# Performance work log

Hardware: AMD Instinct MI355X
Metric: run time of the kernel (lower is better)

Reference implementation:

```python
import jax, jax.numpy as jnp
import numpy as np

B, H, S, D = 2, 16, 2048, 64
DILATION_RATE = 2

def dilated_global_mask(seq_len: int, dilation_rate: int) -> jnp.ndarray:
    # mask[i, j] = 1 if |i - j| % dilation_rate == 0 else 0  -> [S, S] float32
    i = jnp.arange(seq_len)[:, None]
    j = jnp.arange(seq_len)[None, :]
    return ((jnp.abs(i - j) % dilation_rate) == 0).astype(jnp.float32)

def setup_inputs() -> dict:
    key = jax.random.key(0)
    kq, kk, kv = jax.random.split(key, 3)
    queries = jax.random.normal(kq, (B, H, S, D), dtype=jnp.float32)
    keys = jax.random.normal(kk, (B, H, S, D), dtype=jnp.float32)
    values = jax.random.normal(kv, (B, H, S, D), dtype=jnp.float32)
    return {"queries": queries, "keys": keys, "values": values}

def reference(queries, keys, values):
    depth = queries.shape[-1]
    # scores: [B, H, S, S]
    scores = jnp.einsum("bhqd,bhkd->bhqk", queries, keys)
    scores = scores / jnp.sqrt(jnp.asarray(depth, dtype=jnp.float32))
    gmask = dilated_global_mask(keys.shape[-2], DILATION_RATE)  # [S, S]
    # NOTE: multiplicative masking (masked scores become 0, not -inf), as in source
    masked_scores = scores * gmask
    attention_probs = jax.nn.softmax(masked_scores, axis=-1)
    # dropout is identity at inference (training=None)
    out = jnp.einsum("bhqk,bhkd->bhqd", attention_probs, values)
    return out
```

## Files before the change

kernel.cpp:

```cpp
#include <hip/hip_runtime.h>
#include <hip/hip_bf16.h>


#define B_   2
#define H_   16
#define S_   2048
#define D_   64
#define SP_  1024
#define BQ   128
#define BK   64
#define NKT  (SP_ / BK)

#define QSCALE 0.180336884f

typedef __bf16 bf16x8 __attribute__((ext_vector_type(8)));
typedef float  f32x4  __attribute__((ext_vector_type(4)));

#define KSW(r, c8) ((((c8) ^ ((r) & 7)) << 3))

__global__ __launch_bounds__(256, 2) void attn_kernel(const float* __restrict__ Q,
                                                      const float* __restrict__ K,
                                                      const float* __restrict__ V,
                                                      float* __restrict__ out) {
    const int bh  = blockIdx.x;
    const int par = blockIdx.y;
    const int qt  = blockIdx.z;
    const int tid  = threadIdx.x;
    const int lane = tid & 63;
    const int wave = tid >> 6;
    const int l15  = lane & 15;
    const int quad = lane >> 4;

    __shared__ __align__(16) __bf16 kbuf[2][BK][64];
    __shared__ __align__(16) __bf16 vbuf[2][D_][64];
    __shared__ __align__(16) __bf16 p_s[4][16][64];

    const size_t base = (size_t)bh * S_ * D_;
    const float* Qb = Q + base;
    const float* Kb = K + base;
    const float* Vb = V + base;
    const int vofs = (par == 0) ? D_ : -D_;

    bf16x8 qf[2][2];
    #pragma unroll
    for (int mt = 0; mt < 2; ++mt) {
        const int qrow = qt * BQ + wave * 32 + mt * 16 + l15;
        const float* qsrc = Qb + (size_t)(par + 2 * qrow) * D_ + quad * 8;
        #pragma unroll
        for (int ks = 0; ks < 2; ++ks) {
            const float4 a = *(const float4*)(qsrc + ks * 32);
            const float4 b = *(const float4*)(qsrc + ks * 32 + 4);
            bf16x8 w;
            w[0] = (__bf16)(a.x * QSCALE); w[1] = (__bf16)(a.y * QSCALE);
            w[2] = (__bf16)(a.z * QSCALE); w[3] = (__bf16)(a.w * QSCALE);
            w[4] = (__bf16)(b.x * QSCALE); w[5] = (__bf16)(b.y * QSCALE);
            w[6] = (__bf16)(b.z * QSCALE); w[7] = (__bf16)(b.w * QSCALE);
            qf[mt][ks] = w;
        }
    }

    const int kr0 = tid >> 3;
    const int kc8 = tid & 7;

    float4 pka[2], pkb[2];
    float  pv[16], pvo[16];

    #pragma unroll
    for (int i = 0; i < 2; ++i) {
        const int r = i * 32 + kr0;
        const float* ksrc = Kb + (size_t)(par + 2 * r) * D_ + kc8 * 8;
        pka[i] = *(const float4*)ksrc;
        pkb[i] = *(const float4*)(ksrc + 4);
    }
    #pragma unroll
    for (int i = 0; i < 2; ++i) {
        const int c = wave + 4 * i;
        const float* vsrc = Vb + (size_t)(par + 2 * (c * 8)) * D_ + lane;
        #pragma unroll
        for (int j = 0; j < 8; ++j) {
            pv [i * 8 + j] = vsrc[(size_t)(2 * j) * D_];
            pvo[i * 8 + j] = vsrc[(size_t)(2 * j) * D_ + vofs];
        }
    }

    float vo = 0.f;
    #pragma unroll
    for (int i = 0; i < 2; ++i) {
        const int r = i * 32 + kr0;
        bf16x8 w;
        w[0] = (__bf16)pka[i].x; w[1] = (__bf16)pka[i].y;
        w[2] = (__bf16)pka[i].z; w[3] = (__bf16)pka[i].w;
        w[4] = (__bf16)pkb[i].x; w[5] = (__bf16)pkb[i].y;
        w[6] = (__bf16)pkb[i].z; w[7] = (__bf16)pkb[i].w;
        *(bf16x8*)&kbuf[0][r][KSW(r, kc8)] = w;
    }
    #pragma unroll
    for (int i = 0; i < 2; ++i) {
        const int c = wave + 4 * i;
        bf16x8 w;
        #pragma unroll
        for (int j = 0; j < 8; ++j) w[j] = (__bf16)pv[i * 8 + j];
        *(bf16x8*)&vbuf[0][lane][KSW(lane, c)] = w;
        vo += ((pvo[i*8+0] + pvo[i*8+1]) + (pvo[i*8+2] + pvo[i*8+3]))
            + ((pvo[i*8+4] + pvo[i*8+5]) + (pvo[i*8+6] + pvo[i*8+7]));
    }
    __syncthreads();

    f32x4 acc[2][4];
    #pragma unroll
    for (int mt = 0; mt < 2; ++mt)
        #pragma unroll
        for (int nt = 0; nt < 4; ++nt) acc[mt][nt] = (f32x4){0.f, 0.f, 0.f, 0.f};
    float l_acc[2][4] = {{0.f,0.f,0.f,0.f},{0.f,0.f,0.f,0.f}};

    for (int kt = 0; kt < NKT; ++kt) {
        const int cur = kt & 1;
        const bool pf = (kt + 1 < NKT);

        if (pf) {
            #pragma unroll
            for (int i = 0; i < 2; ++i) {
                const int r = i * 32 + kr0;
                const float* ksrc = Kb + (size_t)(par + 2 * ((kt + 1) * BK + r)) * D_ + kc8 * 8;
                pka[i] = *(const float4*)ksrc;
                pkb[i] = *(const float4*)(ksrc + 4);
            }
            #pragma unroll
            for (int i = 0; i < 2; ++i) {
                const int c = wave + 4 * i;
                const float* vsrc = Vb + (size_t)(par + 2 * ((kt + 1) * BK + c * 8)) * D_ + lane;
                #pragma unroll
                for (int j = 0; j < 8; ++j) {
                    pv [i * 8 + j] = vsrc[(size_t)(2 * j) * D_];
                    pvo[i * 8 + j] = vsrc[(size_t)(2 * j) * D_ + vofs];
                }
            }
        }

        {
            const __bf16 (*kb)[64] = kbuf[cur];
            const __bf16 (*vb)[64] = vbuf[cur];
            #pragma unroll
            for (int mt = 0; mt < 2; ++mt) {
                f32x4 sc[4];
                #pragma unroll
                for (int nt = 0; nt < 4; ++nt) sc[nt] = (f32x4){0.f, 0.f, 0.f, 0.f};
                #pragma unroll
                for (int ks = 0; ks < 2; ++ks) {
                    const bf16x8 a = qf[mt][ks];
                    #pragma unroll
                    for (int nt = 0; nt < 4; ++nt) {
                        const int R = nt * 16 + l15;
                        const bf16x8 b = *(const bf16x8*)&kb[R][KSW(R, ks * 4 + quad)];
                        sc[nt] = __builtin_amdgcn_mfma_f32_16x16x32_bf16(a, b, sc[nt], 0, 0, 0);
                    }
                }
                #pragma unroll
                for (int nt = 0; nt < 4; ++nt) {
                    const int colw = ((((nt + quad) & 3) << 4) + l15);
                    #pragma unroll
                    for (int r = 0; r < 4; ++r) {
                        const float p = exp2f(sc[nt][r]);
                        l_acc[mt][r] += p;
                        p_s[wave][quad * 4 + r][colw] = (__bf16)p;
                    }
                }
                #pragma unroll
                for (int ks = 0; ks < 2; ++ks) {
                    const int col0 = ((((2 * ks + (quad >> 1) + (l15 >> 2)) & 3) << 4)
                                      + ((quad & 1) << 3));
                    const bf16x8 pa = *(const bf16x8*)&p_s[wave][l15][col0];
                    #pragma unroll
                    for (int nt = 0; nt < 4; ++nt) {
                        const int R = nt * 16 + l15;
                        const bf16x8 bv = *(const bf16x8*)&vb[R][KSW(R, ks * 4 + quad)];
                        acc[mt][nt] = __builtin_amdgcn_mfma_f32_16x16x32_bf16(pa, bv, acc[mt][nt], 0, 0, 0);
                    }
                }
            }
        }

        if (pf) {
            const int nxt = 1 - cur;
            #pragma unroll
            for (int i = 0; i < 2; ++i) {
                const int r = i * 32 + kr0;
                bf16x8 w;
                w[0] = (__bf16)pka[i].x; w[1] = (__bf16)pka[i].y;
                w[2] = (__bf16)pka[i].z; w[3] = (__bf16)pka[i].w;
                w[4] = (__bf16)pkb[i].x; w[5] = (__bf16)pkb[i].y;
                w[6] = (__bf16)pkb[i].z; w[7] = (__bf16)pkb[i].w;
                *(bf16x8*)&kbuf[nxt][r][KSW(r, kc8)] = w;
            }
            #pragma unroll
            for (int i = 0; i < 2; ++i) {
                const int c = wave + 4 * i;
                bf16x8 w;
                #pragma unroll
                for (int j = 0; j < 8; ++j) w[j] = (__bf16)pv[i * 8 + j];
                *(bf16x8*)&vbuf[nxt][lane][KSW(lane, c)] = w;
                vo += ((pvo[i*8+0] + pvo[i*8+1]) + (pvo[i*8+2] + pvo[i*8+3]))
                    + ((pvo[i*8+4] + pvo[i*8+5]) + (pvo[i*8+6] + pvo[i*8+7]));
            }
        }
        __syncthreads();
    }

    float* vred = (float*)p_s;
    vred[wave * 64 + lane] = vo;
    __syncthreads();

    float rz[2][4];
    #pragma unroll
    for (int mt = 0; mt < 2; ++mt)
        #pragma unroll
        for (int r = 0; r < 4; ++r) {
            float s = l_acc[mt][r];
            #pragma unroll
            for (int off = 1; off < 16; off <<= 1) s += __shfl_xor(s, off);
            rz[mt][r] = 1.0f / (s + 1024.0f);
        }

    #pragma unroll
    for (int nt = 0; nt < 4; ++nt) {
        const int d = nt * 16 + l15;
        const float vso = (vred[d] + vred[64 + d]) + (vred[128 + d] + vred[192 + d]);
        #pragma unroll
        for (int mt = 0; mt < 2; ++mt) {
            #pragma unroll
            for (int r = 0; r < 4; ++r) {
                const int qg = par + 2 * (qt * BQ + wave * 32 + mt * 16 + quad * 4 + r);
                out[base + (size_t)qg * D_ + d] = (acc[mt][nt][r] + vso) * rz[mt][r];
            }
        }
    }
}

extern "C" void kernel_launch(void* const* d_in, const int* in_sizes, int n_in,
                              void* d_out, int out_size, void* d_ws, size_t ws_size,
                              hipStream_t stream) {
    const float* Q = (const float*)d_in[0];
    const float* K = (const float*)d_in[1];
    const float* V = (const float*)d_in[2];
    float* out = (float*)d_out;
    attn_kernel<<<dim3(B_ * H_, 2, SP_ / BQ), dim3(256), 0, stream>>>(Q, K, V, out);
}
```

Measured before the change: 128.7 us.

## Compute transposed S tiles, hoist K fragments, and share V loads across query tiles

The kernel now computes S^T = K·Q^T, so each lane holds scores for a single query row, which reduces the row-sum to two cross-quad shuffles. K fragments are loaded once per tile and reused for both query sub-tiles. The P tile for both sub-tiles is written to LDS before the PV stage, so each V fragment read is shared by two MFMAs instead of being reloaded per sub-tile. It also swaps exp2f for the hardware exp2 builtin and enlarges the P scratch buffer, which increases register and LDS pressure.

```diff
diff --git a/kernel.cpp b/kernel.cpp
--- a/kernel.cpp
+++ b/kernel.cpp
@@ -10,10 +10,18 @@
 #define BQ   128
 #define BK   64
 #define NKT  (SP_ / BK)
+#define NW   4
 
 #define QSCALE 0.180336884f
 
+#if __has_builtin(__builtin_amdgcn_exp2f)
+#define EXP2(x) __builtin_amdgcn_exp2f(x)
+#else
+#define EXP2(x) exp2f(x)
+#endif
+
 typedef __bf16 bf16x8 __attribute__((ext_vector_type(8)));
+typedef __bf16 bf16x4 __attribute__((ext_vector_type(4)));
 typedef float  f32x4  __attribute__((ext_vector_type(4)));
 
 #define KSW(r, c8) ((((c8) ^ ((r) & 7)) << 3))
@@ -33,7 +41,7 @@
 
     __shared__ __align__(16) __bf16 kbuf[2][BK][64];
     __shared__ __align__(16) __bf16 vbuf[2][D_][64];
-    __shared__ __align__(16) __bf16 p_s[4][16][64];
+    __shared__ __align__(16) __bf16 pt[NW][32][64];
 
     const size_t base = (size_t)bh * S_ * D_;
     const float* Qb = Q + base;
@@ -43,8 +51,8 @@
 
     bf16x8 qf[2][2];
     #pragma unroll
-    for (int mt = 0; mt < 2; ++mt) {
-        const int qrow = qt * BQ + wave * 32 + mt * 16 + l15;
+    for (int qt2 = 0; qt2 < 2; ++qt2) {
+        const int qrow = qt * BQ + wave * 32 + qt2 * 16 + l15;
         const float* qsrc = Qb + (size_t)(par + 2 * qrow) * D_ + quad * 8;
         #pragma unroll
         for (int ks = 0; ks < 2; ++ks) {
@@ -55,7 +63,7 @@
             w[2] = (__bf16)(a.z * QSCALE); w[3] = (__bf16)(a.w * QSCALE);
             w[4] = (__bf16)(b.x * QSCALE); w[5] = (__bf16)(b.y * QSCALE);
             w[6] = (__bf16)(b.z * QSCALE); w[7] = (__bf16)(b.w * QSCALE);
-            qf[mt][ks] = w;
+            qf[qt2][ks] = w;
         }
     }
 
@@ -65,174 +73,151 @@
     float4 pka[2], pkb[2];
     float  pv[16], pvo[16];
 
-    #pragma unroll
-    for (int i = 0; i < 2; ++i) {
-        const int r = i * 32 + kr0;
-        const float* ksrc = Kb + (size_t)(par + 2 * r) * D_ + kc8 * 8;
-        pka[i] = *(const float4*)ksrc;
-        pkb[i] = *(const float4*)(ksrc + 4);
-    }
-    #pragma unroll
-    for (int i = 0; i < 2; ++i) {
-        const int c = wave + 4 * i;
-        const float* vsrc = Vb + (size_t)(par + 2 * (c * 8)) * D_ + lane;
-        #pragma unroll
-        for (int j = 0; j < 8; ++j) {
-            pv [i * 8 + j] = vsrc[(size_t)(2 * j) * D_];
-            pvo[i * 8 + j] = vsrc[(size_t)(2 * j) * D_ + vofs];
-        }
-    }
+    auto issue_loads = [&](int kt) {
+        #pragma unroll
+        for (int i = 0; i < 2; ++i) {
+            const int r = i * 32 + kr0;
+            const float* ksrc = Kb + (size_t)(par + 2 * (kt * BK + r)) * D_ + kc8 * 8;
+            pka[i] = *(const float4*)ksrc;
+            pkb[i] = *(const float4*)(ksrc + 4);
+        }
+        #pragma unroll
+        for (int i = 0; i < 2; ++i) {
+            const int c = wave + 4 * i;
+            const float* vsrc = Vb + (size_t)(par + 2 * (kt * BK + c * 8)) * D_ + lane;
+            #pragma unroll
+            for (int j = 0; j < 8; ++j) {
+                pv [i * 8 + j] = vsrc[(size_t)(2 * j) * D_];
+                pvo[i * 8 + j] = vsrc[(size_t)(2 * j) * D_ + vofs];
+            }
+        }
+    };
 
     float vo = 0.f;
-    #pragma unroll
-    for (int i = 0; i < 2; ++i) {
-        const int r = i * 32 + kr0;
-        bf16x8 w;
-        w[0] = (__bf16)pka[i].x; w[1] = (__bf16)pka[i].y;
-        w[2] = (__bf16)pka[i].z; w[3] = (__bf16)pka[i].w;
-        w[4] = (__bf16)pkb[i].x; w[5] = (__bf16)pkb[i].y;
-        w[6] = (__bf16)pkb[i].z; w[7] = (__bf16)pkb[i].w;
-        *(bf16x8*)&kbuf[0][r][KSW(r, kc8)] = w;
-    }
-    #pragma unroll
-    for (int i = 0; i < 2; ++i) {
-        const int c = wave + 4 * i;
-        bf16x8 w;
-        #pragma unroll
-        for (int j = 0; j < 8; ++j) w[j] = (__bf16)pv[i * 8 + j];
-        *(bf16x8*)&vbuf[0][lane][KSW(lane, c)] = w;
-        vo += ((pvo[i*8+0] + pvo[i*8+1]) + (pvo[i*8+2] + pvo[i*8+3]))
-            + ((pvo[i*8+4] + pvo[i*8+5]) + (pvo[i*8+6] + pvo[i*8+7]));
-    }
+    auto stage = [&](int buf) {
+        #pragma unroll
+        for (int i = 0; i < 2; ++i) {
+            const int r = i * 32 + kr0;
+            bf16x8 w;
+            w[0] = (__bf16)pka[i].x; w[1] = (__bf16)pka[i].y;
+            w[2] = (__bf16)pka[i].z; w[3] = (__bf16)pka[i].w;
+            w[4] = (__bf16)pkb[i].x; w[5] = (__bf16)pkb[i].y;
+            w[6] = (__bf16)pkb[i].z; w[7] = (__bf16)pkb[i].w;
+            *(bf16x8*)&kbuf[buf][r][KSW(r, kc8)] = w;
+        }
+        #pragma unroll
+        for (int i = 0; i < 2; ++i) {
+            const int c = wave + 4 * i;
+            bf16x8 w;
+            #pragma unroll
+            for (int j = 0; j < 8; ++j) w[j] = (__bf16)pv[i * 8 + j];
+            *(bf16x8*)&vbuf[buf][lane][KSW(lane, c)] = w;
+            vo += ((pvo[i*8+0] + pvo[i*8+1]) + (pvo[i*8+2] + pvo[i*8+3]))
+                + ((pvo[i*8+4] + pvo[i*8+5]) + (pvo[i*8+6] + pvo[i*8+7]));
+        }
+    };
+
+    issue_loads(0);
+    stage(0);
     __syncthreads();
 
     f32x4 acc[2][4];
     #pragma unroll
-    for (int mt = 0; mt < 2; ++mt)
-        #pragma unroll
-        for (int nt = 0; nt < 4; ++nt) acc[mt][nt] = (f32x4){0.f, 0.f, 0.f, 0.f};
-    float l_acc[2][4] = {{0.f,0.f,0.f,0.f},{0.f,0.f,0.f,0.f}};
+    for (int q2 = 0; q2 < 2; ++q2)
+        #pragma unroll
+        for (int dt = 0; dt < 4; ++dt) acc[q2][dt] = (f32x4){0.f, 0.f, 0.f, 0.f};
+    float l_acc[2] = {0.f, 0.f};
 
     for (int kt = 0; kt < NKT; ++kt) {
         const int cur = kt & 1;
         const bool pf = (kt + 1 < NKT);
 
-        if (pf) {
-            #pragma unroll
-            for (int i = 0; i < 2; ++i) {
-                const int r = i * 32 + kr0;
-                const float* ksrc = Kb + (size_t)(par + 2 * ((kt + 1) * BK + r)) * D_ + kc8 * 8;
-                pka[i] = *(const float4*)ksrc;
-                pkb[i] = *(const float4*)(ksrc + 4);
-            }
-            #pragma unroll
-            for (int i = 0; i < 2; ++i) {
-                const int c = wave + 4 * i;
-                const float* vsrc = Vb + (size_t)(par + 2 * ((kt + 1) * BK + c * 8)) * D_ + lane;
+        if (pf) issue_loads(kt + 1);
+
+        const __bf16 (*kb)[64] = kbuf[cur];
+        const __bf16 (*vb)[64] = vbuf[cur];
+
+        bf16x8 ka[2][4];
+        #pragma unroll
+        for (int ks = 0; ks < 2; ++ks)
+            #pragma unroll
+            for (int kt4 = 0; kt4 < 4; ++kt4) {
+                const int R = kt4 * 16 + l15;
+                ka[ks][kt4] = *(const bf16x8*)&kb[R][KSW(R, ks * 4 + quad)];
+            }
+
+        #pragma unroll
+        for (int qt2 = 0; qt2 < 2; ++qt2) {
+            f32x4 st[4];
+            #pragma unroll
+            for (int kt4 = 0; kt4 < 4; ++kt4) st[kt4] = (f32x4){0.f, 0.f, 0.f, 0.f};
+            #pragma unroll
+            for (int ks = 0; ks < 2; ++ks)
                 #pragma unroll
-                for (int j = 0; j < 8; ++j) {
-                    pv [i * 8 + j] = vsrc[(size_t)(2 * j) * D_];
-                    pvo[i * 8 + j] = vsrc[(size_t)(2 * j) * D_ + vofs];
+                for (int kt4 = 0; kt4 < 4; ++kt4)
+                    st[kt4] = __builtin_amdgcn_mfma_f32_16x16x32_bf16(
+                        ka[ks][kt4], qf[qt2][ks], st[kt4], 0, 0, 0);
+            #pragma unroll
+            for (int kt4 = 0; kt4 < 4; ++kt4) {
+                bf16x4 w;
+                #pragma unroll
+                for (int r = 0; r < 4; ++r) {
+                    const float p = EXP2(st[kt4][r]);
+                    l_acc[qt2] += p;
+                    w[r] = (__bf16)p;
                 }
-            }
-        }
-
-        {
-            const __bf16 (*kb)[64] = kbuf[cur];
-            const __bf16 (*vb)[64] = vbuf[cur];
-            #pragma unroll
-            for (int mt = 0; mt < 2; ++mt) {
-                f32x4 sc[4];
-                #pragma unroll
-                for (int nt = 0; nt < 4; ++nt) sc[nt] = (f32x4){0.f, 0.f, 0.f, 0.f};
-                #pragma unroll
-                for (int ks = 0; ks < 2; ++ks) {
-                    const bf16x8 a = qf[mt][ks];
-                    #pragma unroll
-                    for (int nt = 0; nt < 4; ++nt) {
-                        const int R = nt * 16 + l15;
-                        const bf16x8 b = *(const bf16x8*)&kb[R][KSW(R, ks * 4 + quad)];
-                        sc[nt] = __builtin_amdgcn_mfma_f32_16x16x32_bf16(a, b, sc[nt], 0, 0, 0);
-                    }
-                }
-                #pragma unroll
-                for (int nt = 0; nt < 4; ++nt) {
-                    const int colw = ((((nt + quad) & 3) << 4) + l15);
-                    #pragma unroll
-                    for (int r = 0; r < 4; ++r) {
-                        const float p = exp2f(sc[nt][r]);
-                        l_acc[mt][r] += p;
-                        p_s[wave][quad * 4 + r][colw] = (__bf16)p;
-                    }
-                }
-                #pragma unroll
-                for (int ks = 0; ks < 2; ++ks) {
-                    const int col0 = ((((2 * ks + (quad >> 1) + (l15 >> 2)) & 3) << 4)
-                                      + ((quad & 1) << 3));
-                    const bf16x8 pa = *(const bf16x8*)&p_s[wave][l15][col0];
-                    #pragma unroll
-                    for (int nt = 0; nt < 4; ++nt) {
-                        const int R = nt * 16 + l15;
-                        const bf16x8 bv = *(const bf16x8*)&vb[R][KSW(R, ks * 4 + quad)];
-                        acc[mt][nt] = __builtin_amdgcn_mfma_f32_16x16x32_bf16(pa, bv, acc[mt][nt], 0, 0, 0);
-                    }
-                }
-            }
-        }
-
-        if (pf) {
-            const int nxt = 1 - cur;
-            #pragma unroll
-            for (int i = 0; i < 2; ++i) {
-                const int r = i * 32 + kr0;
-                bf16x8 w;
-                w[0] = (__bf16)pka[i].x; w[1] = (__bf16)pka[i].y;
-                w[2] = (__bf16)pka[i].z; w[3] = (__bf16)pka[i].w;
-                w[4] = (__bf16)pkb[i].x; w[5] = (__bf16)pkb[i].y;
-                w[6] = (__bf16)pkb[i].z; w[7] = (__bf16)pkb[i].w;
-                *(bf16x8*)&kbuf[nxt][r][KSW(r, kc8)] = w;
-            }
-            #pragma unroll
-            for (int i = 0; i < 2; ++i) {
-                const int c = wave + 4 * i;
-                bf16x8 w;
-                #pragma unroll
-                for (int j = 0; j < 8; ++j) w[j] = (__bf16)pv[i * 8 + j];
-                *(bf16x8*)&vbuf[nxt][lane][KSW(lane, c)] = w;
-                vo += ((pvo[i*8+0] + pvo[i*8+1]) + (pvo[i*8+2] + pvo[i*8+3]))
-                    + ((pvo[i*8+4] + pvo[i*8+5]) + (pvo[i*8+6] + pvo[i*8+7]));
-            }
-        }
+                const int ch = (kt4 * 2 + (quad >> 1)) ^ (l15 & 7);
+                *(bf16x4*)&pt[wave][qt2 * 16 + l15][ch * 8 + (quad & 1) * 4] = w;
+            }
+        }
+
+        #pragma unroll
+        for (int ks = 0; ks < 2; ++ks) {
+            bf16x8 pa[2];
+            #pragma unroll
+            for (int qt2 = 0; qt2 < 2; ++qt2)
+                pa[qt2] = *(const bf16x8*)
+                    &pt[wave][qt2 * 16 + l15][KSW(l15, ks * 4 + quad)];
+            #pragma unroll
+            for (int dt = 0; dt < 4; ++dt) {
+                const int Rv = dt * 16 + l15;
+                const bf16x8 bv = *(const bf16x8*)&vb[Rv][KSW(Rv, ks * 4 + quad)];
+                acc[0][dt] = __builtin_amdgcn_mfma_f32_16x16x32_bf16(pa[0], bv, acc[0][dt], 0, 0, 0);
+                acc[1][dt] = __builtin_amdgcn_mfma_f32_16x16x32_bf16(pa[1], bv, acc[1][dt], 0, 0, 0);
+            }
+        }
+
+        if (pf) stage(1 - cur);
         __syncthreads();
     }
 
-    float* vred = (float*)p_s;
+    float* vred = (float*)pt;
     vred[wave * 64 + lane] = vo;
     __syncthreads();
 
     float rz[2][4];
     #pragma unroll
-    for (int mt = 0; mt < 2; ++mt)
+    for (int qt2 = 0; qt2 < 2; ++qt2) {
+        float lf = l_acc[qt2];
+        lf += __shfl_xor(lf, 16);
+        lf += __shfl_xor(lf, 32);
         #pragma unroll
         for (int r = 0; r < 4; ++r) {
-            float s = l_acc[mt][r];
-            #pragma unroll
-            for (int off = 1; off < 16; off <<= 1) s += __shfl_xor(s, off);
-            rz[mt][r] = 1.0f / (s + 1024.0f);
-        }
-
-    #pragma unroll
-    for (int nt = 0; nt < 4; ++nt) {
-        const int d = nt * 16 + l15;
+            const float lr = __shfl(lf, quad * 4 + r);
+            rz[qt2][r] = 1.0f / (lr + 1024.0f);
+        }
+    }
+    #pragma unroll
+    for (int dt = 0; dt < 4; ++dt) {
+        const int d = dt * 16 + l15;
         const float vso = (vred[d] + vred[64 + d]) + (vred[128 + d] + vred[192 + d]);
         #pragma unroll
-        for (int mt = 0; mt < 2; ++mt) {
+        for (int qt2 = 0; qt2 < 2; ++qt2)
             #pragma unroll
             for (int r = 0; r < 4; ++r) {
-                const int qg = par + 2 * (qt * BQ + wave * 32 + mt * 16 + quad * 4 + r);
-                out[base + (size_t)qg * D_ + d] = (acc[mt][nt][r] + vso) * rz[mt][r];
-            }
-        }
+                const int qg = par + 2 * (qt * BQ + wave * 32 + qt2 * 16 + quad * 4 + r);
+                out[base + (size_t)qg * D_ + d] = (acc[qt2][dt][r] + vso) * rz[qt2][r];
+            }
     }
 }
 
```

Result: faster. 113.8 us (-11.6%).
